# Optimization experiments

Measured on AMD Instinct MI355X. Metric: run time of the kernel, lower is better.

The kernel has to match this reference:

```python
import jax, jax.numpy as jnp
import numpy as np

EPS = 1e-6  # annotated-transformer LayerNorm eps


def setup_inputs() -> dict:
    key = jax.random.key(0)
    ks = jax.random.split(key, 6)
    B, S, D, F, G_dom = 32, 512, 1024, 2048, 4
    x = jax.random.normal(ks[0], (B, S, D), dtype=jnp.float32)
    # disjoint partition of the batch into 4 equal domain groups (like the
    # per-domain LongTensor index lists in the torch forward)
    perm = jax.random.permutation(ks[1], B).astype(jnp.int32)
    idx = perm.reshape(G_dom, B // G_dom)  # [4, 8]
    s1 = 1.0 / np.sqrt(D)
    s2 = 1.0 / np.sqrt(F)
    W1 = jax.random.normal(ks[2], (G_dom, D, F), dtype=jnp.float32) * s1
    B1 = jnp.zeros((G_dom, F), dtype=jnp.float32)
    W2 = jax.random.normal(ks[3], (G_dom, F, D), dtype=jnp.float32) * s2
    B2 = jnp.zeros((G_dom, D), dtype=jnp.float32)
    G = jnp.ones((G_dom, D), dtype=jnp.float32)
    Bn = jnp.zeros((G_dom, D), dtype=jnp.float32)
    return {"x": x, "idx": idx, "W1": W1, "B1": B1, "W2": W2, "B2": B2,
            "G": G, "Bn": Bn}


def _layer_norm(x, g, b):
    # matches torch: a_2 * (x - mean) / (std + eps) + b_2, std unbiased (ddof=1)
    mu = jnp.mean(x, axis=-1, keepdims=True)
    sd = jnp.std(x, axis=-1, keepdims=True, ddof=1)
    return g * (x - mu) / (sd + EPS) + b


def reference(x, idx, W1, B1, W2, B2, G, Bn):
    # gather per-domain token groups: [n_dom, per_dom, S, D]
    xg = x[idx]
    # SublayerConnection (eval mode, dropout off): x + adapter(norm(x))
    h = _layer_norm(xg, G[:, None, None, :], Bn[:, None, None, :])
    h = jax.nn.relu(jnp.einsum('gbsd,gdf->gbsf', h, W1) + B1[:, None, None, :])
    a = jnp.einsum('gbsf,gfd->gbsd', h, W2) + B2[:, None, None, :]
    out_g = xg + a
    # scatter combine (index_copy): indices are a disjoint partition
    S_, D_ = x.shape[1], x.shape[2]
    out = jnp.zeros_like(x).at[idx.reshape(-1)].set(out_g.reshape(-1, S_, D_))
    return out
```

## Files before the change

kernel.cpp:

```cpp
#include <hip/hip_runtime.h>
#include <hip/hip_bf16.h>


#define S_DIM 512
#define D_DIM 1024
#define F_DIM 2048
#define MPG   4096

typedef __attribute__((ext_vector_type(8))) short  short8;
typedef __attribute__((ext_vector_type(4))) float  f32x4;

__device__ __forceinline__ void gll16(const void* g, void* l) {
  __builtin_amdgcn_global_load_lds((__attribute__((address_space(1))) void*)g,
                                   (__attribute__((address_space(3))) void*)l,
                                   16, 0, 0);
}
#define VMC0()  asm volatile("s_waitcnt vmcnt(0)" ::: "memory")
#define SB()    __builtin_amdgcn_sched_barrier(0)
#define BAR()   __builtin_amdgcn_s_barrier()

__global__ __launch_bounds__(256) void prep_kernel(
    const float* __restrict__ W1, const float* __restrict__ W2,
    const float* __restrict__ x,  const int* __restrict__ idx,
    const float* __restrict__ G,  const float* __restrict__ Bn,
    __hip_bfloat16* __restrict__ W1t, __hip_bfloat16* __restrict__ W2t,
    __hip_bfloat16* __restrict__ Xn)
{
  __shared__ float tl[32][33];
  const int bid = blockIdx.x;
  if (bid < 16384) {
    const float* src; __hip_bfloat16* dst;
    int R, C, tr, tc;
    if (bid < 8192) {
      const int g = bid >> 11, t = bid & 2047;
      R = 1024; C = 2048; tr = t >> 6; tc = t & 63;
      src = W1 + (size_t)g * R * C;
      dst = W1t + (size_t)g * R * C;
    } else {
      const int b2 = bid - 8192;
      const int g = b2 >> 11, t = b2 & 2047;
      R = 2048; C = 1024; tr = t >> 5; tc = t & 31;
      src = W2 + (size_t)g * R * C;
      dst = W2t + (size_t)g * R * C;
    }
    const int tx = threadIdx.x & 31, ty = threadIdx.x >> 5;
    const int r0 = tr * 32, c0 = tc * 32;
#pragma unroll
    for (int i = 0; i < 4; ++i)
      tl[ty + 8 * i][tx] = src[(size_t)(r0 + ty + 8 * i) * C + (c0 + tx)];
    __syncthreads();
#pragma unroll
    for (int i = 0; i < 4; ++i)
      dst[(size_t)(c0 + ty + 8 * i) * R + (r0 + tx)] = __float2bfloat16(tl[tx][ty + 8 * i]);
    return;
  }
  const int lb   = bid - 16384;
  const int wid  = lb * 4 + (threadIdx.x >> 6);
  const int lane = threadIdx.x & 63;
  const int g = wid >> 12;
  const int r = wid & 4095;
  const int j = r >> 9;
  const int tok = r & 511;
  const int b = idx[g * 8 + j];

  const float* src = x + ((size_t)b * S_DIM + tok) * D_DIM + lane * 16;
  float4 vq[4];
#pragma unroll
  for (int i = 0; i < 4; ++i) vq[i] = ((const float4*)src)[i];
  const float* va = (const float*)vq;

  float s = 0.f, s2 = 0.f;
#pragma unroll
  for (int i = 0; i < 16; ++i) { s += va[i]; s2 += va[i] * va[i]; }
#pragma unroll
  for (int o = 32; o > 0; o >>= 1) { s += __shfl_xor(s, o); s2 += __shfl_xor(s2, o); }

  const float mu  = s * (1.0f / 1024.0f);
  float var = fmaxf(s2 * (1.0f / 1024.0f) - mu * mu, 0.0f) * (1024.0f / 1023.0f);
  const float rs  = 1.0f / (sqrtf(var) + 1e-6f);

  float4 gq[4], bq[4];
  const float* gp = G  + (size_t)g * D_DIM + lane * 16;
  const float* bp = Bn + (size_t)g * D_DIM + lane * 16;
#pragma unroll
  for (int i = 0; i < 4; ++i) { gq[i] = ((const float4*)gp)[i]; bq[i] = ((const float4*)bp)[i]; }
  const float* ga = (const float*)gq;
  const float* be = (const float*)bq;

  __align__(16) __hip_bfloat16 ob[16];
#pragma unroll
  for (int i = 0; i < 16; ++i)
    ob[i] = __float2bfloat16(ga[i] * (va[i] - mu) * rs + be[i]);

  __hip_bfloat16* dst = Xn + ((size_t)g * MPG + r) * D_DIM + lane * 16;
  ((uint4*)dst)[0] = *(const uint4*)&ob[0];
  ((uint4*)dst)[1] = *(const uint4*)&ob[8];
}

template <bool SECOND>
__global__ __launch_bounds__(512, 2) void gemm_kernel(
    const __hip_bfloat16* __restrict__ A,
    const __hip_bfloat16* __restrict__ Bw,
    const float* __restrict__ bias,
    const float* __restrict__ xres,
    const int* __restrict__ idx,
    __hip_bfloat16* __restrict__ obf,
    float* __restrict__ of32,
    const int N, const int K, const int NT)
{
  extern __shared__ char lds[];
  const int ntile = N >> 8;
  const int nwg = gridDim.x;
  const int bid0 = blockIdx.x;
  const int bid = (bid0 & 7) * (nwg >> 3) + (bid0 >> 3);
  const int mt = bid / ntile, nt = bid % ntile;
  const int g  = mt >> 4;
  const int tid = threadIdx.x;
  const int w = tid >> 6, lane = tid & 63;
  const int wm = w >> 2, wn = w & 3;

  const __hip_bfloat16* Ab = A + (size_t)mt * 256 * K;
  const __hip_bfloat16* Bb = Bw + ((size_t)g * N + (size_t)nt * 256) * K;

  const int sp   = (lane & 7) ^ ((lane >> 3) & 7);
  const int srow = 2 * (lane >> 3) + (sp >> 2);
  const int skof = (sp & 3) * 8;
  const __hip_bfloat16* Ag0 = Ab + (size_t)(w * 32 + srow) * K + skof;
  const __hip_bfloat16* Ag1 = Ag0 + (size_t)16 * K;
  const __hip_bfloat16* Bg0 = Bb + (size_t)(w * 32 + srow) * K + skof;
  const __hip_bfloat16* Bg1 = Bg0 + (size_t)16 * K;

  const int l15 = lane & 15, sl = lane >> 4;
  const int slot_phys = (((l15 & 1) << 2) + sl) ^ ((l15 >> 1) & 7);
  const int lane_c = ((l15 >> 1) << 7) + (slot_phys << 4);

  f32x4 acc[8][4] = {};
  short8 frA[2][4], frB[2][4];

#define STAGE4(BUFX, TN) {                                                  \
    const int k0 = (TN) * 64;                                               \
    char* d0 = lds + (BUFX) + w * 2048;                                     \
    gll16(Ag0 + k0,      d0);         gll16(Ag1 + k0,      d0 + 1024);      \
    gll16(Bg0 + k0,      d0 + 16384); gll16(Bg1 + k0,      d0 + 17408);     \
    gll16(Ag0 + k0 + 32, d0 + 32768); gll16(Ag1 + k0 + 32, d0 + 33792);     \
    gll16(Bg0 + k0 + 32, d0 + 49152); gll16(Bg1 + k0 + 32, d0 + 50176); }

#define RDA2(BUFB, MH) {                                                    \
    _Pragma("unroll") for (int kh = 0; kh < 2; ++kh) {                      \
      const char* b_ = lds + (BUFB) + kh * 32768 + wm * 8192 +              \
                       (MH) * 4096 + lane_c;                                \
      _Pragma("unroll") for (int mm = 0; mm < 4; ++mm)                      \
        frA[kh][mm] = *(const short8*)(b_ + mm * 1024); } }

#define RDB2(BUFB) {                                                        \
    _Pragma("unroll") for (int kh = 0; kh < 2; ++kh) {                      \
      const char* b_ = lds + (BUFB) + 16384 + kh * 32768 + wn * 4096 +      \
                       lane_c;                                              \
      _Pragma("unroll") for (int n = 0; n < 4; ++n)                         \
        frB[kh][n] = *(const short8*)(b_ + n * 1024); } }

#define MF32(MH) {                                                          \
    __builtin_amdgcn_s_setprio(1);                                          \
    _Pragma("unroll") for (int kh = 0; kh < 2; ++kh)                        \
      _Pragma("unroll") for (int mm = 0; mm < 4; ++mm)                      \
        _Pragma("unroll") for (int n = 0; n < 4; ++n)                       \
          acc[(MH) * 4 + mm][n] = __builtin_amdgcn_mfma_f32_16x16x32_bf16(  \
              frA[kh][mm], frB[kh][n], acc[(MH) * 4 + mm][n], 0, 0, 0);     \
    __builtin_amdgcn_s_setprio(0); }

  STAGE4(0, 0);

  for (int t = 0; t < NT; ++t) {
    const int bufb = (t & 1) << 16;
    const int bufx = bufb ^ 65536;
    VMC0();
    BAR();
    SB();
    RDB2(bufb);
    RDA2(bufb, 0);
    MF32(0);
    if (t + 1 < NT) STAGE4(bufx, t + 1);
    RDA2(bufb, 1);
    MF32(1);
  }
#undef STAGE4
#undef RDA2
#undef RDB2
#undef MF32

  const int cc  = lane & 15;
  const int cr4 = (lane >> 4) * 4;

  float bv[4];
#pragma unroll
  for (int n = 0; n < 4; ++n)
    bv[n] = bias[(size_t)g * N + nt * 256 + wn * 64 + n * 16 + cc];

  float* wsl = (float*)(lds + w * 4352);
  const int rr  = lane >> 3;
  const int c8  = (lane & 7) * 8;
  const int gcol0 = nt * 256 + wn * 64 + c8;

  if constexpr (!SECOND) {
#pragma unroll
    for (int p = 0; p < 8; ++p) {
#pragma unroll
      for (int n = 0; n < 4; ++n)
#pragma unroll
        for (int i = 0; i < 4; ++i)
          wsl[(cr4 + i) * 68 + n * 16 + cc] = fmaxf(acc[p][n][i] + bv[n], 0.0f);
      const int grow0 = mt * 256 + wm * 128 + p * 16;
#pragma unroll
      for (int it = 0; it < 2; ++it) {
        const int r = it * 8 + rr;
        float4 v0 = *(const float4*)&wsl[r * 68 + c8];
        float4 v1 = *(const float4*)&wsl[r * 68 + c8 + 4];
        __align__(16) __hip_bfloat16 ob[8];
        ob[0] = __float2bfloat16(v0.x); ob[1] = __float2bfloat16(v0.y);
        ob[2] = __float2bfloat16(v0.z); ob[3] = __float2bfloat16(v0.w);
        ob[4] = __float2bfloat16(v1.x); ob[5] = __float2bfloat16(v1.y);
        ob[6] = __float2bfloat16(v1.z); ob[7] = __float2bfloat16(v1.w);
        *(uint4*)&obf[(size_t)(grow0 + r) * N + gcol0] = *(const uint4*)ob;
      }
    }
  } else {
    const int rbase = (mt & 15) * 256;
    const int b = idx[g * 8 + (rbase >> 9)];
    const size_t ob = (size_t)b * S_DIM * D_DIM;
#pragma unroll
    for (int p = 0; p < 8; ++p) {
#pragma unroll
      for (int n = 0; n < 4; ++n)
#pragma unroll
        for (int i = 0; i < 4; ++i)
          wsl[(cr4 + i) * 68 + n * 16 + cc] = acc[p][n][i] + bv[n];
      const int rloc0 = rbase + wm * 128 + p * 16;
#pragma unroll
      for (int it = 0; it < 2; ++it) {
        const int r = it * 8 + rr;
        const int tok = (rloc0 + r) & 511;
        const size_t off = ob + (size_t)tok * D_DIM + gcol0;
        float4 v0 = *(const float4*)&wsl[r * 68 + c8];
        float4 v1 = *(const float4*)&wsl[r * 68 + c8 + 4];
        float4 x0 = *(const float4*)&xres[off];
        float4 x1 = *(const float4*)&xres[off + 4];
        v0.x += x0.x; v0.y += x0.y; v0.z += x0.z; v0.w += x0.w;
        v1.x += x1.x; v1.y += x1.y; v1.z += x1.z; v1.w += x1.w;
        *(float4*)&of32[off]     = v0;
        *(float4*)&of32[off + 4] = v1;
      }
    }
  }
}

extern "C" void kernel_launch(void* const* d_in, const int* in_sizes, int n_in,
                              void* d_out, int out_size, void* d_ws, size_t ws_size,
                              hipStream_t stream) {
  const float* x  = (const float*)d_in[0];
  const int*   idx = (const int*)d_in[1];
  const float* W1 = (const float*)d_in[2];
  const float* B1 = (const float*)d_in[3];
  const float* W2 = (const float*)d_in[4];
  const float* B2 = (const float*)d_in[5];
  const float* G  = (const float*)d_in[6];
  const float* Bn = (const float*)d_in[7];
  float* out = (float*)d_out;

  char* ws = (char*)d_ws;
  __hip_bfloat16* Xn  = (__hip_bfloat16*)(ws);
  __hip_bfloat16* W1t = (__hip_bfloat16*)(ws + 33554432);
  __hip_bfloat16* W2t = (__hip_bfloat16*)(ws + 50331648);
  __hip_bfloat16* H1  = (__hip_bfloat16*)(ws + 67108864);

  (void)hipFuncSetAttribute((const void*)gemm_kernel<false>,
                            hipFuncAttributeMaxDynamicSharedMemorySize, 131072);
  (void)hipFuncSetAttribute((const void*)gemm_kernel<true>,
                            hipFuncAttributeMaxDynamicSharedMemorySize, 131072);

  prep_kernel<<<dim3(20480), dim3(256), 0, stream>>>(
      W1, W2, x, idx, G, Bn, W1t, W2t, Xn);
  gemm_kernel<false><<<dim3(512), dim3(512), 131072, stream>>>(
      Xn, W1t, B1, nullptr, nullptr, H1, nullptr, F_DIM, D_DIM, 16);
  gemm_kernel<true><<<dim3(256), dim3(512), 131072, stream>>>(
      H1, W2t, B2, x, idx, nullptr, out, D_DIM, F_DIM, 32);
}
```

Baseline: 171.3 us.

## Halve GEMM K-step and use 256x128 tiles for second GEMM

The GEMM kernel is templated on N tile width. Its K step per stage drops from 64 to 32, which halves LDS per buffer so both GEMMs need far less shared memory and more workgroups can sit on each CU. The second GEMM switches to 256x128 tiles, doubling its grid from 256 to 512 workgroups to fill more CUs. A barrier is added before the epilogue because it reuses LDS. In exchange there are twice as many loop iterations and barriers, and the narrower tile reuses A less.

```diff
diff --git a/kernel.cpp b/kernel.cpp
--- a/kernel.cpp
+++ b/kernel.cpp
@@ -97,7 +97,7 @@
   ((uint4*)dst)[1] = *(const uint4*)&ob[8];
 }
 
-template <bool SECOND>
+template <int BN_, bool SECOND>
 __global__ __launch_bounds__(512, 2) void gemm_kernel(
     const __hip_bfloat16* __restrict__ A,
     const __hip_bfloat16* __restrict__ Bw,
@@ -108,8 +108,14 @@
     float* __restrict__ of32,
     const int N, const int K, const int NT)
 {
+  constexpr int APL  = 16384;
+  constexpr int BPL  = BN_ * 64;
+  constexpr int BUF  = APL + BPL;
+  constexpr int NFR  = BN_ / 64;
+  constexpr int BROWS = BN_ / 8;
+
   extern __shared__ char lds[];
-  const int ntile = N >> 8;
+  const int ntile = N / BN_;
   const int nwg = gridDim.x;
   const int bid0 = blockIdx.x;
   const int bid = (bid0 & 7) * (nwg >> 3) + (bid0 >> 3);
@@ -120,99 +126,98 @@
   const int wm = w >> 2, wn = w & 3;
 
   const __hip_bfloat16* Ab = A + (size_t)mt * 256 * K;
-  const __hip_bfloat16* Bb = Bw + ((size_t)g * N + (size_t)nt * 256) * K;
+  const __hip_bfloat16* Bb = Bw + ((size_t)g * N + (size_t)nt * BN_) * K;
 
   const int sp   = (lane & 7) ^ ((lane >> 3) & 7);
   const int srow = 2 * (lane >> 3) + (sp >> 2);
   const int skof = (sp & 3) * 8;
   const __hip_bfloat16* Ag0 = Ab + (size_t)(w * 32 + srow) * K + skof;
   const __hip_bfloat16* Ag1 = Ag0 + (size_t)16 * K;
-  const __hip_bfloat16* Bg0 = Bb + (size_t)(w * 32 + srow) * K + skof;
+  const __hip_bfloat16* Bg0 = Bb + (size_t)(w * BROWS + srow) * K + skof;
   const __hip_bfloat16* Bg1 = Bg0 + (size_t)16 * K;
 
   const int l15 = lane & 15, sl = lane >> 4;
   const int slot_phys = (((l15 & 1) << 2) + sl) ^ ((l15 >> 1) & 7);
   const int lane_c = ((l15 >> 1) << 7) + (slot_phys << 4);
 
-  f32x4 acc[8][4] = {};
-  short8 frA[2][4], frB[2][4];
-
-#define STAGE4(BUFX, TN) {                                                  \
-    const int k0 = (TN) * 64;                                               \
-    char* d0 = lds + (BUFX) + w * 2048;                                     \
-    gll16(Ag0 + k0,      d0);         gll16(Ag1 + k0,      d0 + 1024);      \
-    gll16(Bg0 + k0,      d0 + 16384); gll16(Bg1 + k0,      d0 + 17408);     \
-    gll16(Ag0 + k0 + 32, d0 + 32768); gll16(Ag1 + k0 + 32, d0 + 33792);     \
-    gll16(Bg0 + k0 + 32, d0 + 49152); gll16(Bg1 + k0 + 32, d0 + 50176); }
-
-#define RDA2(BUFB, MH) {                                                    \
-    _Pragma("unroll") for (int kh = 0; kh < 2; ++kh) {                      \
-      const char* b_ = lds + (BUFB) + kh * 32768 + wm * 8192 +              \
-                       (MH) * 4096 + lane_c;                                \
-      _Pragma("unroll") for (int mm = 0; mm < 4; ++mm)                      \
-        frA[kh][mm] = *(const short8*)(b_ + mm * 1024); } }
-
-#define RDB2(BUFB) {                                                        \
-    _Pragma("unroll") for (int kh = 0; kh < 2; ++kh) {                      \
-      const char* b_ = lds + (BUFB) + 16384 + kh * 32768 + wn * 4096 +      \
-                       lane_c;                                              \
-      _Pragma("unroll") for (int n = 0; n < 4; ++n)                         \
-        frB[kh][n] = *(const short8*)(b_ + n * 1024); } }
-
-#define MF32(MH) {                                                          \
+  f32x4 acc[8][NFR] = {};
+  short8 frA[4], frB[NFR];
+
+#define STAGE(BUFX, TN) {                                                   \
+    const int k0 = (TN) * 32;                                               \
+    char* dA = lds + (BUFX) + w * 2048;                                     \
+    gll16(Ag0 + k0, dA); gll16(Ag1 + k0, dA + 1024);                        \
+    char* dB = lds + (BUFX) + APL + w * (BROWS * 64);                       \
+    gll16(Bg0 + k0, dB);                                                    \
+    if (BN_ == 256) gll16(Bg1 + k0, dB + 1024); }
+
+#define RDA(BUFB, MH) {                                                     \
+    const char* b_ = lds + (BUFB) + wm * 8192 + (MH) * 4096 + lane_c;       \
+    _Pragma("unroll") for (int mm = 0; mm < 4; ++mm)                        \
+      frA[mm] = *(const short8*)(b_ + mm * 1024); }
+
+#define RDB(BUFB) {                                                         \
+    const char* b_ = lds + (BUFB) + APL + wn * (BPL / 4) + lane_c;          \
+    _Pragma("unroll") for (int n = 0; n < NFR; ++n)                         \
+      frB[n] = *(const short8*)(b_ + n * 1024); }
+
+#define MF(MH) {                                                            \
     __builtin_amdgcn_s_setprio(1);                                          \
-    _Pragma("unroll") for (int kh = 0; kh < 2; ++kh)                        \
-      _Pragma("unroll") for (int mm = 0; mm < 4; ++mm)                      \
-        _Pragma("unroll") for (int n = 0; n < 4; ++n)                       \
-          acc[(MH) * 4 + mm][n] = __builtin_amdgcn_mfma_f32_16x16x32_bf16(  \
-              frA[kh][mm], frB[kh][n], acc[(MH) * 4 + mm][n], 0, 0, 0);     \
+    _Pragma("unroll") for (int mm = 0; mm < 4; ++mm)                        \
+      _Pragma("unroll") for (int n = 0; n < NFR; ++n)                       \
+        acc[(MH) * 4 + mm][n] = __builtin_amdgcn_mfma_f32_16x16x32_bf16(    \
+            frA[mm], frB[n], acc[(MH) * 4 + mm][n], 0, 0, 0);               \
     __builtin_amdgcn_s_setprio(0); }
 
-  STAGE4(0, 0);
+  STAGE(0, 0);
 
   for (int t = 0; t < NT; ++t) {
-    const int bufb = (t & 1) << 16;
-    const int bufx = bufb ^ 65536;
+    const int bufb = (t & 1) ? BUF : 0;
+    const int bufx = (t & 1) ? 0 : BUF;
     VMC0();
     BAR();
     SB();
-    RDB2(bufb);
-    RDA2(bufb, 0);
-    MF32(0);
-    if (t + 1 < NT) STAGE4(bufx, t + 1);
-    RDA2(bufb, 1);
-    MF32(1);
+    RDB(bufb);
+    RDA(bufb, 0);
+    MF(0);
+    if (t + 1 < NT) STAGE(bufx, t + 1);
+    RDA(bufb, 1);
+    MF(1);
   }
-#undef STAGE4
-#undef RDA2
-#undef RDB2
-#undef MF32
+#undef STAGE
+#undef RDA
+#undef RDB
+#undef MF
+
+  BAR();
 
   const int cc  = lane & 15;
   const int cr4 = (lane >> 4) * 4;
 
-  float bv[4];
-#pragma unroll
-  for (int n = 0; n < 4; ++n)
-    bv[n] = bias[(size_t)g * N + nt * 256 + wn * 64 + n * 16 + cc];
+  float bv[NFR];
+#pragma unroll
+  for (int n = 0; n < NFR; ++n)
+    bv[n] = bias[(size_t)g * N + nt * BN_ + wn * (BN_ / 4) + n * 16 + cc];
 
   float* wsl = (float*)(lds + w * 4352);
-  const int rr  = lane >> 3;
-  const int c8  = (lane & 7) * 8;
-  const int gcol0 = nt * 256 + wn * 64 + c8;
+  constexpr int CG  = BN_ / 32;
+  constexpr int RIT = CG / 4;
+  const int rr  = lane / CG;
+  const int c8  = (lane % CG) * 8;
+  const int gcol0 = nt * BN_ + wn * (BN_ / 4) + c8;
 
   if constexpr (!SECOND) {
 #pragma unroll
     for (int p = 0; p < 8; ++p) {
 #pragma unroll
-      for (int n = 0; n < 4; ++n)
+      for (int n = 0; n < NFR; ++n)
 #pragma unroll
         for (int i = 0; i < 4; ++i)
           wsl[(cr4 + i) * 68 + n * 16 + cc] = fmaxf(acc[p][n][i] + bv[n], 0.0f);
       const int grow0 = mt * 256 + wm * 128 + p * 16;
 #pragma unroll
-      for (int it = 0; it < 2; ++it) {
-        const int r = it * 8 + rr;
+      for (int it = 0; it < RIT; ++it) {
+        const int r = it * (64 / CG) + rr;
         float4 v0 = *(const float4*)&wsl[r * 68 + c8];
         float4 v1 = *(const float4*)&wsl[r * 68 + c8 + 4];
         __align__(16) __hip_bfloat16 ob[8];
@@ -230,14 +235,14 @@
 #pragma unroll
     for (int p = 0; p < 8; ++p) {
 #pragma unroll
-      for (int n = 0; n < 4; ++n)
+      for (int n = 0; n < NFR; ++n)
 #pragma unroll
         for (int i = 0; i < 4; ++i)
           wsl[(cr4 + i) * 68 + n * 16 + cc] = acc[p][n][i] + bv[n];
       const int rloc0 = rbase + wm * 128 + p * 16;
 #pragma unroll
-      for (int it = 0; it < 2; ++it) {
-        const int r = it * 8 + rr;
+      for (int it = 0; it < RIT; ++it) {
+        const int r = it * (64 / CG) + rr;
         const int tok = (rloc0 + r) & 511;
         const size_t off = ob + (size_t)tok * D_DIM + gcol0;
         float4 v0 = *(const float4*)&wsl[r * 68 + c8];
@@ -272,15 +277,15 @@
   __hip_bfloat16* W2t = (__hip_bfloat16*)(ws + 50331648);
   __hip_bfloat16* H1  = (__hip_bfloat16*)(ws + 67108864);
 
-  (void)hipFuncSetAttribute((const void*)gemm_kernel<false>,
-                            hipFuncAttributeMaxDynamicSharedMemorySize, 131072);
-  (void)hipFuncSetAttribute((const void*)gemm_kernel<true>,
-                            hipFuncAttributeMaxDynamicSharedMemorySize, 131072);
+  (void)hipFuncSetAttribute((const void*)gemm_kernel<256, false>,
+                            hipFuncAttributeMaxDynamicSharedMemorySize, 65536);
+  (void)hipFuncSetAttribute((const void*)gemm_kernel<128, true>,
+                            hipFuncAttributeMaxDynamicSharedMemorySize, 49152);
 
   prep_kernel<<<dim3(20480), dim3(256), 0, stream>>>(
       W1, W2, x, idx, G, Bn, W1t, W2t, Xn);
-  gemm_kernel<false><<<dim3(512), dim3(512), 131072, stream>>>(
-      Xn, W1t, B1, nullptr, nullptr, H1, nullptr, F_DIM, D_DIM, 16);
-  gemm_kernel<true><<<dim3(256), dim3(512), 131072, stream>>>(
-      H1, W2t, B2, x, idx, nullptr, out, D_DIM, F_DIM, 32);
-}
+  gemm_kernel<256, false><<<dim3(512), dim3(512), 65536, stream>>>(
+      Xn, W1t, B1, nullptr, nullptr, H1, nullptr, F_DIM, D_DIM, 32);
+  gemm_kernel<128, true><<<dim3(512), dim3(512), 49152, stream>>>(
+      H1, W2t, B2, x, idx, nullptr, out, D_DIM, F_DIM, 64);
+}
```

New measurement: 187.8 us, median of 2. 1.1x slower.

## Switch GEMM inner loop to 32x32x16 bf16 MFMA with matching epilogue

Applied to the files above, without the earlier changes.

Replaces the 16x16x32 MFMA tiling with 32x32x16 bf16 MFMA instructions, changing fragment loading from LDS, accumulator layout (f32x16) and the epilogue write-back through LDS. Larger MFMA tiles read fewer LDS fragments per FLOP and issue fewer instructions. The epilogue now uses a 33-float padded staging row and writes 16 contiguous columns per lane pair. Risks include LDS bank conflicts in the new swizzle mapping, the unaligned float4 reads from a stride-33 layout, and higher register pressure.

```diff
diff --git a/kernel.cpp b/kernel.cpp
--- a/kernel.cpp
+++ b/kernel.cpp
@@ -7,8 +7,9 @@
 #define F_DIM 2048
 #define MPG   4096
 
-typedef __attribute__((ext_vector_type(8))) short  short8;
-typedef __attribute__((ext_vector_type(4))) float  f32x4;
+typedef __attribute__((ext_vector_type(8)))  short short8;
+typedef __attribute__((ext_vector_type(4)))  float f32x4;
+typedef __attribute__((ext_vector_type(16))) float f32x16;
 
 __device__ __forceinline__ void gll16(const void* g, void* l) {
   __builtin_amdgcn_global_load_lds((__attribute__((address_space(1))) void*)g,
@@ -130,12 +131,14 @@
   const __hip_bfloat16* Bg0 = Bb + (size_t)(w * 32 + srow) * K + skof;
   const __hip_bfloat16* Bg1 = Bg0 + (size_t)16 * K;
 
-  const int l15 = lane & 15, sl = lane >> 4;
-  const int slot_phys = (((l15 & 1) << 2) + sl) ^ ((l15 >> 1) & 7);
-  const int lane_c = ((l15 >> 1) << 7) + (slot_phys << 4);
-
-  f32x4 acc[8][4] = {};
-  short8 frA[2][4], frB[2][4];
+  const int l31 = lane & 31, khalf = lane >> 5;
+  const int sp_lo = (((l31 & 1) << 2) + khalf)     ^ ((l31 >> 1) & 7);
+  const int sp_hi = (((l31 & 1) << 2) + 2 + khalf) ^ ((l31 >> 1) & 7);
+  const int aoff_lo = ((l31 >> 1) << 7) + (sp_lo << 4);
+  const int aoff_hi = ((l31 >> 1) << 7) + (sp_hi << 4);
+
+  f32x16 acc[4][2] = {};
+  short8 fa[2][4], fb[2][4];
 
 #define STAGE4(BUFX, TN) {                                                  \
     const int k0 = (TN) * 64;                                               \
@@ -145,27 +148,29 @@
     gll16(Ag0 + k0 + 32, d0 + 32768); gll16(Ag1 + k0 + 32, d0 + 33792);     \
     gll16(Bg0 + k0 + 32, d0 + 49152); gll16(Bg1 + k0 + 32, d0 + 50176); }
 
-#define RDA2(BUFB, MH) {                                                    \
-    _Pragma("unroll") for (int kh = 0; kh < 2; ++kh) {                      \
-      const char* b_ = lds + (BUFB) + kh * 32768 + wm * 8192 +              \
-                       (MH) * 4096 + lane_c;                                \
-      _Pragma("unroll") for (int mm = 0; mm < 4; ++mm)                      \
-        frA[kh][mm] = *(const short8*)(b_ + mm * 1024); } }
-
-#define RDB2(BUFB) {                                                        \
-    _Pragma("unroll") for (int kh = 0; kh < 2; ++kh) {                      \
-      const char* b_ = lds + (BUFB) + 16384 + kh * 32768 + wn * 4096 +      \
-                       lane_c;                                              \
-      _Pragma("unroll") for (int n = 0; n < 4; ++n)                         \
-        frB[kh][n] = *(const short8*)(b_ + n * 1024); } }
-
-#define MF32(MH) {                                                          \
+#define RDA(BUFB, MH) {                                                     \
+    _Pragma("unroll") for (int m2 = 0; m2 < 2; ++m2)                        \
+      _Pragma("unroll") for (int kc = 0; kc < 4; ++kc) {                    \
+        const char* b_ = lds + (BUFB) + (kc >> 1) * 32768 + wm * 8192 +     \
+                         ((MH) * 2 + m2) * 2048 +                           \
+                         ((kc & 1) ? aoff_hi : aoff_lo);                    \
+        fa[m2][kc] = *(const short8*)b_; } }
+
+#define RDB(BUFB) {                                                         \
+    _Pragma("unroll") for (int n2 = 0; n2 < 2; ++n2)                        \
+      _Pragma("unroll") for (int kc = 0; kc < 4; ++kc) {                    \
+        const char* b_ = lds + (BUFB) + 16384 + (kc >> 1) * 32768 +         \
+                         wn * 4096 + n2 * 2048 +                            \
+                         ((kc & 1) ? aoff_hi : aoff_lo);                    \
+        fb[n2][kc] = *(const short8*)b_; } }
+
+#define MF(MH) {                                                            \
     __builtin_amdgcn_s_setprio(1);                                          \
-    _Pragma("unroll") for (int kh = 0; kh < 2; ++kh)                        \
-      _Pragma("unroll") for (int mm = 0; mm < 4; ++mm)                      \
-        _Pragma("unroll") for (int n = 0; n < 4; ++n)                       \
-          acc[(MH) * 4 + mm][n] = __builtin_amdgcn_mfma_f32_16x16x32_bf16(  \
-              frA[kh][mm], frB[kh][n], acc[(MH) * 4 + mm][n], 0, 0, 0);     \
+    _Pragma("unroll") for (int kc = 0; kc < 4; ++kc)                        \
+      _Pragma("unroll") for (int m2 = 0; m2 < 2; ++m2)                      \
+        _Pragma("unroll") for (int n2 = 0; n2 < 2; ++n2)                    \
+          acc[(MH) * 2 + m2][n2] = __builtin_amdgcn_mfma_f32_32x32x16_bf16( \
+              fa[m2][kc], fb[n2][kc], acc[(MH) * 2 + m2][n2], 0, 0, 0);     \
     __builtin_amdgcn_s_setprio(0); }
 
   STAGE4(0, 0);
@@ -176,78 +181,82 @@
     VMC0();
     BAR();
     SB();
-    RDB2(bufb);
-    RDA2(bufb, 0);
-    MF32(0);
+    RDB(bufb);
+    RDA(bufb, 0);
+    MF(0);
     if (t + 1 < NT) STAGE4(bufx, t + 1);
-    RDA2(bufb, 1);
-    MF32(1);
+    RDA(bufb, 1);
+    MF(1);
   }
 #undef STAGE4
-#undef RDA2
-#undef RDB2
-#undef MF32
-
-  const int cc  = lane & 15;
-  const int cr4 = (lane >> 4) * 4;
-
-  float bv[4];
-#pragma unroll
-  for (int n = 0; n < 4; ++n)
-    bv[n] = bias[(size_t)g * N + nt * 256 + wn * 64 + n * 16 + cc];
+#undef RDA
+#undef RDB
+#undef MF
+
+  BAR();
 
   float* wsl = (float*)(lds + w * 4352);
-  const int rr  = lane >> 3;
-  const int c8  = (lane & 7) * 8;
-  const int gcol0 = nt * 256 + wn * 64 + c8;
-
-  if constexpr (!SECOND) {
-#pragma unroll
-    for (int p = 0; p < 8; ++p) {
-#pragma unroll
-      for (int n = 0; n < 4; ++n)
-#pragma unroll
-        for (int i = 0; i < 4; ++i)
-          wsl[(cr4 + i) * 68 + n * 16 + cc] = fmaxf(acc[p][n][i] + bv[n], 0.0f);
-      const int grow0 = mt * 256 + wm * 128 + p * 16;
-#pragma unroll
-      for (int it = 0; it < 2; ++it) {
-        const int r = it * 8 + rr;
-        float4 v0 = *(const float4*)&wsl[r * 68 + c8];
-        float4 v1 = *(const float4*)&wsl[r * 68 + c8 + 4];
-        __align__(16) __hip_bfloat16 ob[8];
-        ob[0] = __float2bfloat16(v0.x); ob[1] = __float2bfloat16(v0.y);
-        ob[2] = __float2bfloat16(v0.z); ob[3] = __float2bfloat16(v0.w);
-        ob[4] = __float2bfloat16(v1.x); ob[5] = __float2bfloat16(v1.y);
-        ob[6] = __float2bfloat16(v1.z); ob[7] = __float2bfloat16(v1.w);
-        *(uint4*)&obf[(size_t)(grow0 + r) * N + gcol0] = *(const uint4*)ob;
+  const int rr2 = lane >> 1;
+  const int cb  = (lane & 1) * 16;
+
+  float bvv[2];
+#pragma unroll
+  for (int n2 = 0; n2 < 2; ++n2)
+    bvv[n2] = bias[(size_t)g * N + nt * 256 + wn * 64 + n2 * 32 + l31];
+
+  const int rbase = (mt & 15) * 256;
+  const int bsc = SECOND ? idx[g * 8 + (rbase >> 9)] : 0;
+  const size_t obase = (size_t)bsc * S_DIM * D_DIM;
+
+#pragma unroll
+  for (int m2 = 0; m2 < 4; ++m2) {
+#pragma unroll
+    for (int n2 = 0; n2 < 2; ++n2) {
+#pragma unroll
+      for (int rg = 0; rg < 16; ++rg) {
+        const int row = (rg & 3) + 8 * (rg >> 2) + 4 * khalf;
+        float v = acc[m2][n2][rg] + bvv[n2];
+        if (!SECOND) v = fmaxf(v, 0.0f);
+        wsl[row * 33 + l31] = v;
       }
-    }
-  } else {
-    const int rbase = (mt & 15) * 256;
-    const int b = idx[g * 8 + (rbase >> 9)];
-    const size_t ob = (size_t)b * S_DIM * D_DIM;
-#pragma unroll
-    for (int p = 0; p < 8; ++p) {
-#pragma unroll
-      for (int n = 0; n < 4; ++n)
-#pragma unroll
-        for (int i = 0; i < 4; ++i)
-          wsl[(cr4 + i) * 68 + n * 16 + cc] = acc[p][n][i] + bv[n];
-      const int rloc0 = rbase + wm * 128 + p * 16;
-#pragma unroll
-      for (int it = 0; it < 2; ++it) {
-        const int r = it * 8 + rr;
-        const int tok = (rloc0 + r) & 511;
-        const size_t off = ob + (size_t)tok * D_DIM + gcol0;
-        float4 v0 = *(const float4*)&wsl[r * 68 + c8];
-        float4 v1 = *(const float4*)&wsl[r * 68 + c8 + 4];
+      const int gcol = nt * 256 + wn * 64 + n2 * 32 + cb;
+      if constexpr (!SECOND) {
+        const int grow = mt * 256 + wm * 128 + m2 * 32 + rr2;
+        float4 v0 = *(const float4*)&wsl[rr2 * 33 + cb];
+        float4 v1 = *(const float4*)&wsl[rr2 * 33 + cb + 4];
+        float4 v2 = *(const float4*)&wsl[rr2 * 33 + cb + 8];
+        float4 v3 = *(const float4*)&wsl[rr2 * 33 + cb + 12];
+        __align__(16) __hip_bfloat16 ob[16];
+        ob[0]=__float2bfloat16(v0.x); ob[1]=__float2bfloat16(v0.y);
+        ob[2]=__float2bfloat16(v0.z); ob[3]=__float2bfloat16(v0.w);
+        ob[4]=__float2bfloat16(v1.x); ob[5]=__float2bfloat16(v1.y);
+        ob[6]=__float2bfloat16(v1.z); ob[7]=__float2bfloat16(v1.w);
+        ob[8]=__float2bfloat16(v2.x); ob[9]=__float2bfloat16(v2.y);
+        ob[10]=__float2bfloat16(v2.z); ob[11]=__float2bfloat16(v2.w);
+        ob[12]=__float2bfloat16(v3.x); ob[13]=__float2bfloat16(v3.y);
+        ob[14]=__float2bfloat16(v3.z); ob[15]=__float2bfloat16(v3.w);
+        *(uint4*)&obf[(size_t)grow * N + gcol]     = *(const uint4*)&ob[0];
+        *(uint4*)&obf[(size_t)grow * N + gcol + 8] = *(const uint4*)&ob[8];
+      } else {
+        const int rloc = rbase + wm * 128 + m2 * 32 + rr2;
+        const int tok = rloc & 511;
+        const size_t off = obase + (size_t)tok * D_DIM + gcol;
+        float4 v0 = *(const float4*)&wsl[rr2 * 33 + cb];
+        float4 v1 = *(const float4*)&wsl[rr2 * 33 + cb + 4];
+        float4 v2 = *(const float4*)&wsl[rr2 * 33 + cb + 8];
+        float4 v3 = *(const float4*)&wsl[rr2 * 33 + cb + 12];
         float4 x0 = *(const float4*)&xres[off];
         float4 x1 = *(const float4*)&xres[off + 4];
-        v0.x += x0.x; v0.y += x0.y; v0.z += x0.z; v0.w += x0.w;
-        v1.x += x1.x; v1.y += x1.y; v1.z += x1.z; v1.w += x1.w;
-        *(float4*)&of32[off]     = v0;
-        *(float4*)&of32[off + 4] = v1;
+        float4 x2 = *(const float4*)&xres[off + 8];
+        float4 x3 = *(const float4*)&xres[off + 12];
+        v0.x+=x0.x; v0.y+=x0.y; v0.z+=x0.z; v0.w+=x0.w;
+        v1.x+=x1.x; v1.y+=x1.y; v1.z+=x1.z; v1.w+=x1.w;
+        v2.x+=x2.x; v2.y+=x2.y; v2.z+=x2.z; v2.w+=x2.w;
+        v3.x+=x3.x; v3.y+=x3.y; v3.z+=x3.z; v3.w+=x3.w;
+        *(float4*)&of32[off]      = v0;
+        *(float4*)&of32[off + 4]  = v1;
+        *(float4*)&of32[off + 8]  = v2;
+        *(float4*)&of32[off + 12] = v3;
       }
     }
   }
```

Result: slower. 217.1 us (+26.7%).
